# Optimization experiments

Measured on AMD Instinct MI355X. Metric: run time of the kernel, lower is better.

## Reference

```python
import jax, jax.numpy as jnp
import numpy as np

B, N, C = 4, 2048, 320
H, D = 5, 64            # heads, dim_head
INNER = H * D           # 320


def setup_inputs() -> dict:
    key = jax.random.key(0)
    ks = jax.random.split(key, 7)
    x = jax.random.normal(ks[0], (B, N, C), dtype=jnp.float32)
    edge = jax.random.uniform(ks[1], (B, N, 1), dtype=jnp.float32)
    s = 1.0 / np.sqrt(C)
    Wq = jax.random.normal(ks[2], (C, INNER), dtype=jnp.float32) * s
    Wk = jax.random.normal(ks[3], (C, INNER), dtype=jnp.float32) * s
    Wv = jax.random.normal(ks[4], (C, INNER), dtype=jnp.float32) * s
    Wo = jax.random.normal(ks[5], (INNER, C), dtype=jnp.float32) * (1.0 / np.sqrt(INNER))
    bo = jnp.zeros((C,), dtype=jnp.float32)
    return {"x": x, "edge": edge, "Wq": Wq, "Wk": Wk, "Wv": Wv, "Wo": Wo, "bo": bo}


def _split_heads(t):
    # 'b n (h d) -> (b h) n d'  (batch-major, head-minor)
    b, n, _ = t.shape
    return t.reshape(b, n, H, D).transpose(0, 2, 1, 3).reshape(b * H, n, D)


def reference(x, edge, Wq, Wk, Wv, Wo, bo):
    scale = D ** -0.5
    q = _split_heads(x @ Wq).astype(jnp.float32)   # (B*H, N, D)
    k = _split_heads(x @ Wk).astype(jnp.float32)
    v = _split_heads(x @ Wv)

    sim = jnp.einsum('bid,bjd->bij', q, k) * scale  # (B*H, N, N)

    # torch: edge.repeat(h, 1, 1) -> batch-minor tiling; index i uses edge[i % B]
    edge_rep = jnp.tile(edge, (H, 1, 1))            # (H*B, N, 1)
    edge_matrix = edge_rep * edge_rep.transpose(0, 2, 1)  # outer product (H*B, N, N)

    sim = jax.nn.softmax(sim * edge_matrix, axis=-1)
    out = jnp.einsum('bij,bjd->bid', sim, v)        # (B*H, N, D)

    # '(b h) n d -> b n (h d)'
    out = out.reshape(B, H, N, D).transpose(0, 2, 1, 3).reshape(B, N, INNER)
    return out @ Wo + bo
```

## Files before the change

### kernel.cpp

```cpp
#include <hip/hip_runtime.h>
#include <hip/hip_bf16.h>
#include <math.h>


typedef short bf16x8 __attribute__((ext_vector_type(8)));
typedef float f32x4 __attribute__((ext_vector_type(4)));

static __device__ __forceinline__ ushort f2bf(float f) {
  union { float f; unsigned u; } v; v.f = f;
  unsigned r = (v.u + 0x7fffu + ((v.u >> 16) & 1u)) >> 16;
  return (ushort)r;
}
static __device__ __forceinline__ float fexp2(float x) {
#if __has_builtin(__builtin_amdgcn_exp2f)
  return __builtin_amdgcn_exp2f(x);
#else
  return exp2f(x);
#endif
}
static __device__ __forceinline__ f32x4 mfma32(bf16x8 a, bf16x8 b, f32x4 c) {
  return __builtin_amdgcn_mfma_f32_16x16x32_bf16(a, b, c, 0, 0, 0);
}

__global__ __launch_bounds__(256) void prep_kernel(
    const float* __restrict__ x,
    const float* __restrict__ Wq, const float* __restrict__ Wk,
    const float* __restrict__ Wv, const float* __restrict__ Wo,
    ushort* __restrict__ xb, ushort* __restrict__ wt)
{
  const int w = blockIdx.x;
  if (w < 2560) {
    const int t = threadIdx.x;
    const int mt2 = w / 5;
    const int kc = (w % 5) * 2 + (t >> 7);
    const int f = (t & 127) * 4;
    const int qq = f >> 7, mm = (f >> 3) & 15, e0 = f & 7;
    float4 v = *reinterpret_cast<const float4*>(
        x + (size_t)(mt2 * 16 + mm) * 320 + kc * 32 + qq * 8 + e0);
    ushort4 o = { f2bf(v.x), f2bf(v.y), f2bf(v.z), f2bf(v.w) };
    *reinterpret_cast<ushort4*>(xb + (size_t)(mt2 * 10 + kc) * 512 + f) = o;
  } else {
    const int w2 = w - 2560;
    const int nt2 = w2 % 20, kc = (w2 / 20) % 10, z = w2 / 200;
    const float* W = z == 0 ? Wq : z == 1 ? Wk : z == 2 ? Wv : Wo;
    const int f = threadIdx.x * 2;
    const int qq = f >> 7, nn = (f >> 3) & 15, e0 = f & 7;
    const int k = kc * 32 + qq * 8 + e0, n = nt2 * 16 + nn;
    float v0 = W[(size_t)k * 320 + n];
    float v1 = W[(size_t)(k + 1) * 320 + n];
    ushort2 o = { f2bf(v0), f2bf(v1) };
    *reinterpret_cast<ushort2*>(
        wt + (size_t)z * 102400 + (size_t)(nt2 * 10 + kc) * 512 + f) = o;
  }
}

__global__ __launch_bounds__(256, 3) void qkv_gemm(
    const ushort* __restrict__ xb, const float* __restrict__ edge,
    const ushort* __restrict__ wt,
    ushort* __restrict__ qp, ushort* __restrict__ kS, ushort* __restrict__ vS)
{
  const int w = blockIdx.x;
  const int s = (w & 7) * 60 + (w >> 3);
  const int mg = s / 15, zh = s % 15;
  const int z = zh / 5, h = zh % 5;
  const int wave = threadIdx.x >> 6, lane = threadIdx.x & 63;
  const int m16 = lane & 15, quad = lane >> 4;
  const int m0 = mg * 256 + wave * 64;
  const ushort* atile = xb + (size_t)(m0 >> 4) * 5120 + lane * 8;
  const ushort* btile = wt + (size_t)z * 102400 + (size_t)(h * 4) * 5120 + lane * 8;

  f32x4 acc[4][4];
#pragma unroll
  for (int i = 0; i < 4; ++i)
#pragma unroll
    for (int ns = 0; ns < 4; ++ns) acc[i][ns] = (f32x4){0.f, 0.f, 0.f, 0.f};

#pragma unroll
  for (int kc = 0; kc < 10; ++kc) {
    bf16x8 af[4], bf[4];
#pragma unroll
    for (int i = 0; i < 4; ++i)
      af[i] = *reinterpret_cast<const bf16x8*>(atile + (i * 10 + kc) * 512);
#pragma unroll
    for (int ns = 0; ns < 4; ++ns)
      bf[ns] = *reinterpret_cast<const bf16x8*>(btile + (ns * 10 + kc) * 512);
    if (z == 2) {
#pragma unroll
      for (int i = 0; i < 4; ++i)
#pragma unroll
        for (int ns = 0; ns < 4; ++ns)
          acc[i][ns] = mfma32(af[i], bf[ns], acc[i][ns]);
    } else {
#pragma unroll
      for (int i = 0; i < 4; ++i)
#pragma unroll
        for (int ns = 0; ns < 4; ++ns)
          acc[i][ns] = mfma32(bf[ns], af[i], acc[i][ns]);
    }
  }

  const float QSCALE = 0.18033688011112042f;
  const int b = m0 >> 11;
  const int bh = b * 5 + h;
  const float* eb = edge + (size_t)((b + h) & 3) * 2048;
  const int nwb = m0 & 2047;

  if (z == 0) {
#pragma unroll
    for (int i = 0; i < 4; ++i) {
      const int n = nwb + i * 16 + m16;
      const float e = eb[n] * QSCALE;
      ushort* dst = qp + ((size_t)bh * 2048 + n) * 64 + quad * 4;
#pragma unroll
      for (int ns = 0; ns < 4; ++ns) {
        ushort4 o = { f2bf(acc[i][ns][0] * e), f2bf(acc[i][ns][1] * e),
                      f2bf(acc[i][ns][2] * e), f2bf(acc[i][ns][3] * e) };
        *reinterpret_cast<ushort4*>(dst + ns * 16) = o;
      }
    }
  } else if (z == 1) {
#pragma unroll
    for (int i = 0; i < 4; ++i) {
      const int j = nwb + i * 16 + m16;
      const float e = eb[j];
      const size_t base = (size_t)bh * 131072 +
                          (size_t)((m0 >> 4) + i & 127) * 1024;
#pragma unroll
      for (int ns = 0; ns < 4; ++ns) {
        size_t a0 = base + (ns >> 1) * 512 +
                    ((((ns * 2 + (quad >> 1)) & 3) * 16 + m16)) * 8 +
                    (quad & 1) * 4;
        ushort4 o = { f2bf(acc[i][ns][0] * e), f2bf(acc[i][ns][1] * e),
                      f2bf(acc[i][ns][2] * e), f2bf(acc[i][ns][3] * e) };
        *reinterpret_cast<ushort4*>(kS + a0) = o;
      }
    }
  } else {
    const int jb = nwb >> 6;
#pragma unroll
    for (int i = 0; i < 4; ++i) {
      const int kb = i >> 1, e4 = (i & 1) * 4;
#pragma unroll
      for (int ns = 0; ns < 4; ++ns) {
        ushort4 o = { f2bf(acc[i][ns][0]), f2bf(acc[i][ns][1]),
                      f2bf(acc[i][ns][2]), f2bf(acc[i][ns][3]) };
        size_t addr = (size_t)bh * 131072 + (size_t)ns * 32768 +
                      (size_t)jb * 1024 + kb * 512 +
                      (quad * 16 + m16) * 8 + e4;
        *reinterpret_cast<ushort4*>(vS + addr) = o;
      }
    }
  }
}

__global__ __launch_bounds__(256, 3) void attn_kernel(
    const ushort* __restrict__ qp, const ushort* __restrict__ kS,
    const ushort* __restrict__ vS, ushort* __restrict__ ao)
{
  __shared__ f32x4 lo[3][8][64];
  __shared__ float lrs[4][2][16];
  const int w = blockIdx.x;
  const int s = (w & 7) * 160 + (w >> 3);
  const int bh = s >> 6, qt = s & 63;
  const int b = bh / 5, h = bh % 5;
  const int wave = threadIdx.x >> 6, lane = threadIdx.x & 63;
  const int m16 = lane & 15, quad = lane >> 4;
  const int q0 = qt * 32;

  bf16x8 qf[2][2];
#pragma unroll
  for (int qs = 0; qs < 2; ++qs) {
    const ushort* qrow = qp + ((size_t)bh * 2048 + q0 + qs * 16 + m16) * 64;
    qf[qs][0] = *reinterpret_cast<const bf16x8*>(qrow + quad * 8);
    qf[qs][1] = *reinterpret_cast<const bf16x8*>(qrow + 32 + quad * 8);
  }
  const ushort* kb_p = kS + (size_t)bh * 131072 + lane * 8;
  const ushort* vb_p = vS + (size_t)bh * 131072 + lane * 8;

  f32x4 oacc[2][4], rsacc[2];
#pragma unroll
  for (int qs = 0; qs < 2; ++qs) {
    rsacc[qs] = (f32x4){0.f, 0.f, 0.f, 0.f};
    for (int dt = 0; dt < 4; ++dt) oacc[qs][dt] = (f32x4){0.f, 0.f, 0.f, 0.f};
  }
  const bf16x8 ones8 = {(short)16256, (short)16256, (short)16256, (short)16256,
                        (short)16256, (short)16256, (short)16256, (short)16256};

  auto load_unit = [&](int u, bf16x8 kf[2][2], bf16x8 vf[4]) {
    const int jb = (u >> 1) * 4 + wave, kb = u & 1;
#pragma unroll
    for (int ss = 0; ss < 2; ++ss)
#pragma unroll
      for (int hf = 0; hf < 2; ++hf)
        kf[ss][hf] = *reinterpret_cast<const bf16x8*>(
            kb_p + (size_t)(jb * 4 + kb * 2 + ss) * 1024 + hf * 512);
#pragma unroll
    for (int dt = 0; dt < 4; ++dt)
      vf[dt] = *reinterpret_cast<const bf16x8*>(
          vb_p + (size_t)dt * 32768 + (size_t)jb * 1024 + kb * 512);
  };
  auto compute_unit = [&](bf16x8 kf[2][2], bf16x8 vf[4]) {
#pragma unroll
    for (int qs = 0; qs < 2; ++qs) {
      f32x4 st0 = (f32x4){0.f, 0.f, 0.f, 0.f};
      f32x4 st1 = (f32x4){0.f, 0.f, 0.f, 0.f};
      st0 = mfma32(kf[0][0], qf[qs][0], st0);
      st0 = mfma32(kf[0][1], qf[qs][1], st0);
      st1 = mfma32(kf[1][0], qf[qs][0], st1);
      st1 = mfma32(kf[1][1], qf[qs][1], st1);
      unsigned b0 = __float_as_uint(fexp2(st0[0]));
      unsigned b1 = __float_as_uint(fexp2(st0[1]));
      unsigned b2 = __float_as_uint(fexp2(st0[2]));
      unsigned b3 = __float_as_uint(fexp2(st0[3]));
      unsigned b4 = __float_as_uint(fexp2(st1[0]));
      unsigned b5 = __float_as_uint(fexp2(st1[1]));
      unsigned b6 = __float_as_uint(fexp2(st1[2]));
      unsigned b7 = __float_as_uint(fexp2(st1[3]));
      union { unsigned u[4]; bf16x8 v; } pk;
      pk.u[0] = __builtin_amdgcn_perm(b1, b0, 0x07060302u);
      pk.u[1] = __builtin_amdgcn_perm(b3, b2, 0x07060302u);
      pk.u[2] = __builtin_amdgcn_perm(b5, b4, 0x07060302u);
      pk.u[3] = __builtin_amdgcn_perm(b7, b6, 0x07060302u);
      rsacc[qs] = mfma32(ones8, pk.v, rsacc[qs]);
#pragma unroll
      for (int dt = 0; dt < 4; ++dt)
        oacc[qs][dt] = mfma32(vf[dt], pk.v, oacc[qs][dt]);
    }
  };

  bf16x8 kA[2][2], vA[4], kB[2][2], vB[4];
  load_unit(0, kA, vA);
  __builtin_amdgcn_sched_barrier(0);
#pragma unroll
  for (int u = 0; u < 16; u += 2) {
    load_unit(u + 1, kB, vB);
    __builtin_amdgcn_sched_barrier(0);
    compute_unit(kA, vA);
    if (u + 2 < 16) load_unit(u + 2, kA, vA);
    __builtin_amdgcn_sched_barrier(0);
    compute_unit(kB, vB);
    __builtin_amdgcn_sched_barrier(0);
  }

  if (wave > 0) {
#pragma unroll
    for (int qs = 0; qs < 2; ++qs)
#pragma unroll
      for (int dt = 0; dt < 4; ++dt)
        lo[wave - 1][qs * 4 + dt][lane] = oacc[qs][dt];
  }
  if (quad == 0) {
    lrs[wave][0][m16] = rsacc[0][0];
    lrs[wave][1][m16] = rsacc[1][0];
  }
  __syncthreads();
  if (wave == 0) {
#pragma unroll
    for (int qs = 0; qs < 2; ++qs) {
      float inv = 1.0f / (lrs[0][qs][m16] + lrs[1][qs][m16] +
                          lrs[2][qs][m16] + lrs[3][qs][m16]);
      const int mt2 = b * 128 + qt * 2 + qs;
#pragma unroll
      for (int dt = 0; dt < 4; ++dt) {
        f32x4 a = oacc[qs][dt];
        a += lo[0][qs * 4 + dt][lane];
        a += lo[1][qs * 4 + dt][lane];
        a += lo[2][qs * 4 + dt][lane];
        unsigned r0 = f2bf(a[0] * inv), r1 = f2bf(a[1] * inv);
        unsigned r2 = f2bf(a[2] * inv), r3 = f2bf(a[3] * inv);
        uint2 ww;
        ww.x = r0 | (r1 << 16);
        ww.y = r2 | (r3 << 16);
        size_t addr = (size_t)(mt2 * 10 + h * 2 + (dt >> 1)) * 512 +
                      ((((dt & 1) * 2 + (quad >> 1)) * 16 + m16)) * 8 +
                      (quad & 1) * 4;
        *reinterpret_cast<uint2*>(ao + addr) = ww;
      }
    }
  }
}

__global__ __launch_bounds__(256, 3) void oproj_gemm(
    const ushort* __restrict__ ao, const ushort* __restrict__ wt,
    const float* __restrict__ bo, float* __restrict__ out)
{
  const int w = blockIdx.x;
  const int s = (w & 7) * 40 + (w >> 3);
  const int mg = s / 5, ct = s % 5;
  const int wave = threadIdx.x >> 6, lane = threadIdx.x & 63;
  const int m16 = lane & 15, quad = lane >> 4;
  const int m0 = mg * 128 + wave * 32;
  const int n0 = ct * 64;
  const ushort* atile = ao + (size_t)(m0 >> 4) * 5120 + lane * 8;
  const ushort* btile = wt + (size_t)3 * 102400 + (size_t)(ct * 4) * 5120 + lane * 8;

  f32x4 acc[2][4];
#pragma unroll
  for (int i = 0; i < 2; ++i)
#pragma unroll
    for (int ns = 0; ns < 4; ++ns) acc[i][ns] = (f32x4){0.f, 0.f, 0.f, 0.f};

#pragma unroll
  for (int kc = 0; kc < 10; ++kc) {
    bf16x8 af[2], bf[4];
#pragma unroll
    for (int i = 0; i < 2; ++i)
      af[i] = *reinterpret_cast<const bf16x8*>(atile + (i * 10 + kc) * 512);
#pragma unroll
    for (int ns = 0; ns < 4; ++ns)
      bf[ns] = *reinterpret_cast<const bf16x8*>(btile + (ns * 10 + kc) * 512);
#pragma unroll
    for (int i = 0; i < 2; ++i)
#pragma unroll
      for (int ns = 0; ns < 4; ++ns)
        acc[i][ns] = mfma32(bf[ns], af[i], acc[i][ns]);
  }

  float4 bb[4];
#pragma unroll
  for (int ns = 0; ns < 4; ++ns)
    bb[ns] = *reinterpret_cast<const float4*>(bo + n0 + ns * 16 + quad * 4);
#pragma unroll
  for (int i = 0; i < 2; ++i) {
    const int mrow = m0 + i * 16 + m16;
#pragma unroll
    for (int ns = 0; ns < 4; ++ns) {
      float4 o;
      o.x = acc[i][ns][0] + bb[ns].x;
      o.y = acc[i][ns][1] + bb[ns].y;
      o.z = acc[i][ns][2] + bb[ns].z;
      o.w = acc[i][ns][3] + bb[ns].w;
      *reinterpret_cast<float4*>(
          out + (size_t)mrow * 320 + n0 + ns * 16 + quad * 4) = o;
    }
  }
}

extern "C" void kernel_launch(void* const* d_in, const int* in_sizes, int n_in,
                              void* d_out, int out_size, void* d_ws, size_t ws_size,
                              hipStream_t stream) {
  const float* x    = (const float*)d_in[0];
  const float* edge = (const float*)d_in[1];
  const float* Wq   = (const float*)d_in[2];
  const float* Wk   = (const float*)d_in[3];
  const float* Wv   = (const float*)d_in[4];
  const float* Wo   = (const float*)d_in[5];
  const float* bo   = (const float*)d_in[6];
  float* out = (float*)d_out;

  ushort* xb = (ushort*)d_ws;
  ushort* wt = xb + (size_t)8192 * 320;
  ushort* qp = wt + (size_t)4 * 320 * 320;
  ushort* kS = qp + (size_t)20 * 2048 * 64;
  ushort* vS = kS + (size_t)20 * 2048 * 64;
  ushort* ao = vS + (size_t)20 * 2048 * 64;

  prep_kernel<<<3360, 256, 0, stream>>>(x, Wq, Wk, Wv, Wo, xb, wt);
  qkv_gemm<<<480, 256, 0, stream>>>(xb, edge, wt, qp, kS, vS);
  attn_kernel<<<1280, 256, 0, stream>>>(qp, kS, vS, ao);
  oproj_gemm<<<320, 256, 0, stream>>>(ao, wt, bo, out);
}
```

Measured before the change: 124.3 us.

## Double query tile per attention block and replace rowsum MFMA with VALU adds

Each attention block now handles 64 query rows instead of 32, halving the grid and the K/V reads per query. Each wave now takes a contiguous quarter of the key range instead of an interleaved slice. The row-sum MFMA against a ones vector is replaced by scalar adds of the bf16-truncated exponentials, followed by cross-lane shuffles. V loads are single-buffered and interleaved with K prefetch to limit register growth, which risks exposing latency and lowering occupancy.

```diff
diff --git a/kernel.cpp b/kernel.cpp
--- a/kernel.cpp
+++ b/kernel.cpp
@@ -157,51 +157,52 @@
     const ushort* __restrict__ qp, const ushort* __restrict__ kS,
     const ushort* __restrict__ vS, ushort* __restrict__ ao)
 {
-  __shared__ f32x4 lo[3][8][64];
-  __shared__ float lrs[4][2][16];
+  __shared__ f32x4 lo[3][16][64];
+  __shared__ float lrs[4][4][16];
   const int w = blockIdx.x;
-  const int s = (w & 7) * 160 + (w >> 3);
-  const int bh = s >> 6, qt = s & 63;
+  const int s = (w & 7) * 80 + (w >> 3);
+  const int bh = s >> 5, qt = s & 31;
   const int b = bh / 5, h = bh % 5;
   const int wave = threadIdx.x >> 6, lane = threadIdx.x & 63;
   const int m16 = lane & 15, quad = lane >> 4;
-  const int q0 = qt * 32;
-
-  bf16x8 qf[2][2];
-#pragma unroll
-  for (int qs = 0; qs < 2; ++qs) {
+  const int q0 = qt * 64;
+
+  bf16x8 qf[4][2];
+#pragma unroll
+  for (int qs = 0; qs < 4; ++qs) {
     const ushort* qrow = qp + ((size_t)bh * 2048 + q0 + qs * 16 + m16) * 64;
     qf[qs][0] = *reinterpret_cast<const bf16x8*>(qrow + quad * 8);
     qf[qs][1] = *reinterpret_cast<const bf16x8*>(qrow + 32 + quad * 8);
   }
-  const ushort* kb_p = kS + (size_t)bh * 131072 + lane * 8;
-  const ushort* vb_p = vS + (size_t)bh * 131072 + lane * 8;
-
-  f32x4 oacc[2][4], rsacc[2];
-#pragma unroll
-  for (int qs = 0; qs < 2; ++qs) {
-    rsacc[qs] = (f32x4){0.f, 0.f, 0.f, 0.f};
+  const ushort* kb_p = kS + (size_t)bh * 131072 + (size_t)wave * 32768 + lane * 8;
+  const ushort* vb_p = vS + (size_t)bh * 131072 + (size_t)wave * 8192 + lane * 8;
+
+  f32x4 oacc[4][4];
+  float rs[4];
+#pragma unroll
+  for (int qs = 0; qs < 4; ++qs) {
+    rs[qs] = 0.f;
+#pragma unroll
     for (int dt = 0; dt < 4; ++dt) oacc[qs][dt] = (f32x4){0.f, 0.f, 0.f, 0.f};
   }
-  const bf16x8 ones8 = {(short)16256, (short)16256, (short)16256, (short)16256,
-                        (short)16256, (short)16256, (short)16256, (short)16256};
-
-  auto load_unit = [&](int u, bf16x8 kf[2][2], bf16x8 vf[4]) {
-    const int jb = (u >> 1) * 4 + wave, kb = u & 1;
+
+  auto load_k = [&](int u, bf16x8 kf[2][2]) {
 #pragma unroll
     for (int ss = 0; ss < 2; ++ss)
 #pragma unroll
       for (int hf = 0; hf < 2; ++hf)
         kf[ss][hf] = *reinterpret_cast<const bf16x8*>(
-            kb_p + (size_t)(jb * 4 + kb * 2 + ss) * 1024 + hf * 512);
+            kb_p + (size_t)u * 2048 + ss * 1024 + hf * 512);
+  };
+  auto load_v = [&](int u, bf16x8 vf[4]) {
 #pragma unroll
     for (int dt = 0; dt < 4; ++dt)
       vf[dt] = *reinterpret_cast<const bf16x8*>(
-          vb_p + (size_t)dt * 32768 + (size_t)jb * 1024 + kb * 512);
+          vb_p + (size_t)dt * 32768 + (size_t)u * 512);
   };
   auto compute_unit = [&](bf16x8 kf[2][2], bf16x8 vf[4]) {
 #pragma unroll
-    for (int qs = 0; qs < 2; ++qs) {
+    for (int qs = 0; qs < 4; ++qs) {
       f32x4 st0 = (f32x4){0.f, 0.f, 0.f, 0.f};
       f32x4 st1 = (f32x4){0.f, 0.f, 0.f, 0.f};
       st0 = mfma32(kf[0][0], qf[qs][0], st0);
@@ -216,50 +217,69 @@
       unsigned b5 = __float_as_uint(fexp2(st1[1]));
       unsigned b6 = __float_as_uint(fexp2(st1[2]));
       unsigned b7 = __float_as_uint(fexp2(st1[3]));
+      float t0 = __uint_as_float(b0 & 0xffff0000u);
+      float t1 = __uint_as_float(b1 & 0xffff0000u);
+      float t2 = __uint_as_float(b2 & 0xffff0000u);
+      float t3 = __uint_as_float(b3 & 0xffff0000u);
+      float t4 = __uint_as_float(b4 & 0xffff0000u);
+      float t5 = __uint_as_float(b5 & 0xffff0000u);
+      float t6 = __uint_as_float(b6 & 0xffff0000u);
+      float t7 = __uint_as_float(b7 & 0xffff0000u);
+      rs[qs] += ((t0 + t1) + (t2 + t3)) + ((t4 + t5) + (t6 + t7));
       union { unsigned u[4]; bf16x8 v; } pk;
       pk.u[0] = __builtin_amdgcn_perm(b1, b0, 0x07060302u);
       pk.u[1] = __builtin_amdgcn_perm(b3, b2, 0x07060302u);
       pk.u[2] = __builtin_amdgcn_perm(b5, b4, 0x07060302u);
       pk.u[3] = __builtin_amdgcn_perm(b7, b6, 0x07060302u);
-      rsacc[qs] = mfma32(ones8, pk.v, rsacc[qs]);
 #pragma unroll
       for (int dt = 0; dt < 4; ++dt)
         oacc[qs][dt] = mfma32(vf[dt], pk.v, oacc[qs][dt]);
     }
   };
 
-  bf16x8 kA[2][2], vA[4], kB[2][2], vB[4];
-  load_unit(0, kA, vA);
+  bf16x8 kA[2][2], kB[2][2], vf[4];
+  load_k(0, kA);
   __builtin_amdgcn_sched_barrier(0);
 #pragma unroll
   for (int u = 0; u < 16; u += 2) {
-    load_unit(u + 1, kB, vB);
+    load_v(u, vf);
+    load_k(u + 1, kB);
     __builtin_amdgcn_sched_barrier(0);
-    compute_unit(kA, vA);
-    if (u + 2 < 16) load_unit(u + 2, kA, vA);
+    compute_unit(kA, vf);
     __builtin_amdgcn_sched_barrier(0);
-    compute_unit(kB, vB);
+    load_v(u + 1, vf);
+    if (u + 2 < 16) load_k(u + 2, kA);
     __builtin_amdgcn_sched_barrier(0);
+    compute_unit(kB, vf);
+    __builtin_amdgcn_sched_barrier(0);
+  }
+
+#pragma unroll
+  for (int qs = 0; qs < 4; ++qs) {
+    float r = rs[qs];
+    r += __shfl_xor(r, 16, 64);
+    r += __shfl_xor(r, 32, 64);
+    rs[qs] = r;
   }
 
   if (wave > 0) {
 #pragma unroll
-    for (int qs = 0; qs < 2; ++qs)
+    for (int qs = 0; qs < 4; ++qs)
 #pragma unroll
       for (int dt = 0; dt < 4; ++dt)
         lo[wave - 1][qs * 4 + dt][lane] = oacc[qs][dt];
   }
   if (quad == 0) {
-    lrs[wave][0][m16] = rsacc[0][0];
-    lrs[wave][1][m16] = rsacc[1][0];
+#pragma unroll
+    for (int qs = 0; qs < 4; ++qs) lrs[wave][qs][m16] = rs[qs];
   }
   __syncthreads();
   if (wave == 0) {
 #pragma unroll
-    for (int qs = 0; qs < 2; ++qs) {
+    for (int qs = 0; qs < 4; ++qs) {
       float inv = 1.0f / (lrs[0][qs][m16] + lrs[1][qs][m16] +
                           lrs[2][qs][m16] + lrs[3][qs][m16]);
-      const int mt2 = b * 128 + qt * 2 + qs;
+      const int mt2 = b * 128 + qt * 4 + qs;
 #pragma unroll
       for (int dt = 0; dt < 4; ++dt) {
         f32x4 a = oacc[qs][dt];
@@ -357,6 +377,6 @@
 
   prep_kernel<<<3360, 256, 0, stream>>>(x, Wq, Wk, Wv, Wo, xb, wt);
   qkv_gemm<<<480, 256, 0, stream>>>(xb, edge, wt, qp, kS, vS);
-  attn_kernel<<<1280, 256, 0, stream>>>(qp, kS, vS, ao);
+  attn_kernel<<<640, 256, 0, stream>>>(qp, kS, vS, ao);
   oproj_gemm<<<320, 256, 0, stream>>>(ao, wt, bo, out);
 }
```

Result: slower. 204.7 us (+64.7%).
